# Kernel tuning notes

Measured on AMD Instinct MI355X. Metric: run time of the kernel, lower is better.

## Reference

```python
import jax, jax.numpy as jnp
import numpy as np

# TISA RBF basis (helpers l2_dist / rbf_basis in the repo): f_i(d) = a_i * exp(-|b_i| * (d - c_i)^2)

def setup_inputs() -> dict:
    key = jax.random.key(0)
    k = jax.random.split(key, 8)
    B, L, H, D, S, F = 2, 2048, 8, 64, 2, 5
    qs = jax.random.normal(k[0], (B, L, H, D), dtype=jnp.float32)
    ks = jax.random.normal(k[1], (B, L, H, D), dtype=jnp.float32)
    vs = jax.random.normal(k[2], (B, L, H, D), dtype=jnp.float32)
    qs_s = jax.random.uniform(k[3], (B, L, S), dtype=jnp.float32)
    ks_s = jax.random.uniform(k[4], (B, L, S), dtype=jnp.float32)
    a = jax.random.uniform(k[5], (H * F,), dtype=jnp.float32)
    b = jax.random.uniform(k[6], (H * F,), dtype=jnp.float32)
    c = jax.random.normal(k[7], (H * F,), dtype=jnp.float32) * 0.5
    return {"qs": qs, "ks": ks, "vs": vs, "qs_s": qs_s, "ks_s": ks_s, "a": a, "b": b, "c": c}


def _tisa_attention(qs, ks, vs, qs_s, ks_s, a, b, c):
    B, Q, H, D = qs.shape
    F = a.size // H
    aH, bH, cH = (p.reshape(H, F) for p in (a, b, c))
    # pairwise euclidean distance between query and key locations: [B, Q, K]
    diff = qs_s[:, :, None, :] - ks_s[:, None, :, :]
    d = jnp.sqrt(jnp.sum(diff * diff, axis=-1))
    d_ = d[:, None]  # [B, 1, Q, K] broadcast over heads
    # RBF bias summed over F basis functions (small fixed F -> python sum avoids B,H,F,Q,K blowup)
    bias = sum(
        aH[:, f][None, :, None, None]
        * jnp.exp(-jnp.abs(bH[:, f])[None, :, None, None] * (d_ - cH[:, f][None, :, None, None]) ** 2)
        for f in range(F)
    )  # [B, H, Q, K]
    scale = 1.0 / jnp.sqrt(jnp.asarray(D, dtype=qs.dtype))
    scores = jnp.einsum('bqhd,bkhd->bhqk', qs * scale, ks) + bias
    attn = jax.nn.softmax(scores, axis=-1)
    return jnp.einsum('bhqk,bkhd->bqhd', attn, vs)


def reference(qs, ks, vs, qs_s, ks_s, a, b, c):
    # Matches scan_tisa_biased_attention: online-softmax chunking is mathematically
    # identical to a single stable softmax over the full key axis.
    return _tisa_attention(qs, ks, vs, qs_s, ks_s, a, b, c)
```

## Files before the change

### kernel.cpp

```cpp
#include <hip/hip_runtime.h>
#include <cmath>

typedef _Float16 half8 __attribute__((ext_vector_type(8)));
typedef _Float16 half4 __attribute__((ext_vector_type(4)));
typedef _Float16 half2v __attribute__((ext_vector_type(2)));
typedef __fp16 fp16x2 __attribute__((ext_vector_type(2)));
typedef float f32x4 __attribute__((ext_vector_type(4)));
typedef float f32x2 __attribute__((ext_vector_type(2)));

#define B_ 2
#define L_ 2048
#define H_ 8
#define D_ 64
#define S_ 2
#define F_ 5
#define LUTN 2048
#define LSCALE 1448.1547f
#define LOG2E 1.44269504f
#define QSC (0.125f * LOG2E)

#define QOFF 0
#define KOFF 2097152
#define VOFF 4194304
#define SOFFH 6291456
#define WS_NEED 12615680

#define OFF_K0 0
#define OFF_K1 16384
#define OFF_V0 32768
#define OFF_V1 49152
#define OFF_LUT 65536
#define ARENA_SZ 73744
#define SLOTF (16 * 68 + 16)

#define GLOBAL_LOAD_LDS16(g, l)                                                  \
  __builtin_amdgcn_global_load_lds((const __attribute__((address_space(1))) void*)(g), \
                                   (__attribute__((address_space(3))) void*)(l), 16, 0, 0)

#define FAST_SQRT(x) __builtin_amdgcn_sqrtf(x)

__global__ __launch_bounds__(512, 4)
void tisa_preproc(const float* __restrict__ qs, const float* __restrict__ ks,
                  const float* __restrict__ vs, const float* __restrict__ ks_s,
                  _Float16* __restrict__ wsh) {
  __shared__ _Float16 Vl[64 * 72];
  const int t = threadIdx.x;
  const int bid = blockIdx.x;
  const int xcd = bid & 7, slot = bid >> 3;
  const int u = slot & 31;
  const int bh = xcd * 2 + (slot >> 5);
  const size_t base = ((size_t)(bh >> 3) * L_ + (size_t)u * 64) * (H_ * D_) + (size_t)(bh & 7) * D_;

  {
    int row = t >> 3, c = t & 7;
    const float* src = qs + base + (size_t)row * 512 + c * 8;
    f32x4 x0 = ((const f32x4*)src)[0], x1 = ((const f32x4*)src)[1];
    half8 hh;
#pragma unroll
    for (int k = 0; k < 4; ++k) { hh[k] = (_Float16)(x0[k] * QSC); hh[k + 4] = (_Float16)(x1[k] * QSC); }
    *(half8*)&wsh[QOFF + ((size_t)bh * 32 + u) * 4096 + row * 64 + (c ^ (row & 7)) * 8] = hh;
  }
  {
    int tile = t >> 8, row = (t >> 3) & 31, c = t & 7;
    const float* src = ks + base + (size_t)(tile * 32 + row) * 512 + c * 8;
    f32x4 x0 = ((const f32x4*)src)[0], x1 = ((const f32x4*)src)[1];
    half8 hh;
#pragma unroll
    for (int k = 0; k < 4; ++k) { hh[k] = (_Float16)x0[k]; hh[k + 4] = (_Float16)x1[k]; }
    *(half8*)&wsh[KOFF + ((size_t)bh * 64 + u * 2 + tile) * 2048 + row * 64 + (c ^ (row & 7)) * 8] = hh;
  }
  if ((bh & 7) == 0 && t < 32) {
    const int b = bh >> 3;
    const float* src = ks_s + ((size_t)b * L_ + u * 64) * 2 + t * 4;
    float* dst = (float*)(wsh + SOFFH) + ((size_t)b * L_ + u * 64) * 2 + t * 4;
    f32x4 x = *(const f32x4*)src;
    x *= LSCALE;
    *(f32x4*)dst = x;
  }
  {
    int key = t >> 3, seg = t & 7;
    const float* src = vs + base + (size_t)key * 512 + seg * 8;
    f32x4 a0 = ((const f32x4*)src)[0], a1 = ((const f32x4*)src)[1];
    half8 h0;
#pragma unroll
    for (int k = 0; k < 4; ++k) { h0[k] = (_Float16)a0[k]; h0[k + 4] = (_Float16)a1[k]; }
    *(half8*)&Vl[key * 72 + seg * 8] = h0;
  }
  __syncthreads();
  {
    int tile = t >> 8, s = (t >> 3) & 31, cp2 = t & 7;
    int d = 2 * s + (cp2 >> 2), kb = (cp2 & 3) * 8;
    half8 hh;
#pragma unroll
    for (int j = 0; j < 8; ++j) {
      int kpj = kb + j;
      int orig = ((kpj >> 2) & 1) * 16 + (kpj >> 3) * 4 + (kpj & 3);
      hh[j] = Vl[(tile * 32 + orig) * 72 + d];
    }
    *(half8*)&wsh[VOFF + ((size_t)bh * 64 + u * 2 + tile) * 2048 + s * 64 + (cp2 ^ (s & 7)) * 8] = hh;
  }
}

__global__ __launch_bounds__(1024, 8)
void tisa_attn_main(const float* __restrict__ qs_s, const float* __restrict__ ap,
                    const float* __restrict__ bp, const float* __restrict__ cp,
                    const _Float16* __restrict__ wsh, float* __restrict__ out) {
  __shared__ __align__(16) char arena[ARENA_SZ];
  float* LUT = (float*)(arena + OFF_LUT);

  const int t = threadIdx.x;
  const int lane = t & 63;
  const int w = t >> 6;
  const int g = w >> 2;
  const int qw = w & 3;
  const int t2 = t & 255;
  const int quad = lane >> 4;
  const int l16 = lane & 15;

  const int bid = blockIdx.x;
  const int xcd = bid & 7, slot = bid >> 3;
  const int qt = slot & 31;
  const int bh = xcd * 2 + (slot >> 5);
  const int h = bh & 7;
  const int b = bh >> 3;
  const int q0 = qt * 64;

  {
    float af[F_], nb[F_], cf[F_];
#pragma unroll
    for (int f = 0; f < F_; ++f) {
      af[f] = ap[h * F_ + f];
      nb[f] = -fabsf(bp[h * F_ + f]);
      cf[f] = cp[h * F_ + f];
    }
    for (int i = t; i <= LUTN; i += 1024) {
      float d = ((float)i + 0.5f) * (1.0f / LSCALE);
      float s = 0.f;
#pragma unroll
      for (int f = 0; f < F_; ++f) {
        float e = d - cf[f];
        s += af[f] * __expf(nb[f] * (e * e));
      }
      LUT[i] = (s - 8.0f) * LOG2E;
    }
  }

  const float qx = qs_s[((size_t)b * L_ + q0 + qw * 16 + l16) * 2 + 0] * LSCALE;
  const float qy = qs_s[((size_t)b * L_ + q0 + qw * 16 + l16) * 2 + 1] * LSCALE;

  const _Float16* Qt = wsh + QOFF + ((size_t)bh * 32 + qt) * 4096;
  const _Float16* Kbh = wsh + KOFF + (size_t)bh * 64 * 2048;
  const _Float16* Vbh = wsh + VOFF + (size_t)bh * 64 * 2048;
  const float* wsS = (const float*)(wsh + SOFFH);

  const _Float16* ksrc = Kbh + (size_t)(g * 16) * 2048 + t2 * 8;
  const _Float16* vsrc = Vbh + (size_t)(g * 16) * 2048 + t2 * 8;
  const float* sbase = wsS + ((size_t)b * L_ + g * 512 + quad * 4) * 2;

  if (w < 8)
    GLOBAL_LOAD_LDS16(Qt + w * 512 + lane * 8, arena + OFF_K1 + w * 1024);
  GLOBAL_LOAD_LDS16(ksrc, arena + OFF_K0 + g * 4096 + qw * 1024);
  GLOBAL_LOAD_LDS16(vsrc, arena + OFF_V0 + g * 4096 + qw * 1024);
  ksrc += 2048; vsrc += 2048;
  __syncthreads();

  half8 qA[2];
#pragma unroll
  for (int kb = 0; kb < 2; ++kb)
    qA[kb] = *(const half8*)(arena + OFF_K1 + (qw * 16 + l16) * 128 +
                             ((kb * 4 + quad) ^ (l16 & 7)) * 16);
  __syncthreads();

  f32x4 oc[4];
#pragma unroll
  for (int df = 0; df < 4; ++df) oc[df] = (f32x4){0.f, 0.f, 0.f, 0.f};
  f32x4 lsacc = (f32x4){0.f, 0.f, 0.f, 0.f};
  half8 onesv;
#pragma unroll
  for (int j = 0; j < 8; ++j) onesv[j] = (_Float16)1.0f;

  int cur16 = 0;
  for (int it = 0; it < 16; ++it) {
    const int nxt16 = cur16 ^ 16384;
    if (it < 15) {
      GLOBAL_LOAD_LDS16(ksrc, arena + OFF_K0 + nxt16 + g * 4096 + qw * 1024);
      GLOBAL_LOAD_LDS16(vsrc, arena + OFF_V0 + nxt16 + g * 4096 + qw * 1024);
      ksrc += 2048; vsrc += 2048;
    }

    const float* sit = sbase + it * 64;
    f32x4 c01a = *(const f32x4*)(sit);
    f32x4 c23a = *(const f32x4*)(sit + 4);
    f32x4 c01b = *(const f32x4*)(sit + 32);
    f32x4 c23b = *(const f32x4*)(sit + 36);

    f32x4 acc[2];
#pragma unroll
    for (int nf = 0; nf < 2; ++nf) {
      f32x4 a = (f32x4){0.f, 0.f, 0.f, 0.f};
#pragma unroll
      for (int kb = 0; kb < 2; ++kb) {
        half8 kf = *(const half8*)(arena + OFF_K0 + cur16 + g * 4096 + (nf * 16 + l16) * 128 +
                                   ((kb * 4 + quad) ^ (l16 & 7)) * 16);
        a = __builtin_amdgcn_mfma_f32_16x16x32_f16(kf, qA[kb], a, 0, 0, 0);
      }
      acc[nf] = a;
    }

    float parr[8];
#pragma unroll
    for (int nf = 0; nf < 2; ++nf) {
      f32x4 cA = (nf == 0) ? c01a : c01b;
      f32x4 cB = (nf == 0) ? c23a : c23b;
      float kxr[4] = {cA.x, cA.z, cB.x, cB.z};
      float kyr[4] = {cA.y, cA.w, cB.y, cB.w};
#pragma unroll
      for (int r = 0; r < 4; ++r) {
        float dx = qx - kxr[r], dy = qy - kyr[r];
        float tt = FAST_SQRT(fmaf(dx, dx, dy * dy));
        int ii = (int)tt;
        parr[nf * 4 + r] = __builtin_amdgcn_exp2f(acc[nf][r] + LUT[ii]);
      }
    }
    union { half8 h8; fp16x2 h2[4]; } pu;
#pragma unroll
    for (int k = 0; k < 4; ++k)
      pu.h2[k] = __builtin_amdgcn_cvt_pkrtz(parr[2 * k], parr[2 * k + 1]);
    half8 pw = pu.h8;

    lsacc = __builtin_amdgcn_mfma_f32_16x16x32_f16(pw, onesv, lsacc, 0, 0, 0);
#pragma unroll
    for (int df = 0; df < 4; ++df) {
      half8 vf = *(const half8*)(arena + OFF_V0 + cur16 + g * 4096 + (l16 >> 1) * 128 + df * 1024 +
                                 ((((l16 & 1) * 4 + quad) ^ ((l16 >> 1) & 7)) * 16));
      oc[df] = __builtin_amdgcn_mfma_f32_16x16x32_f16(pw, vf, oc[df], 0, 0, 0);
    }

    __syncthreads();
    cur16 = nxt16;
  }

  float lred[4];
#pragma unroll
  for (int r = 0; r < 4; ++r) lred[r] = lsacc[r];
  __syncthreads();
  float* slots = (float*)arena;
  if (g >= 2) {
    float* sl = slots + ((g - 2) * 4 + qw) * SLOTF;
#pragma unroll
    for (int df = 0; df < 4; ++df)
#pragma unroll
      for (int r = 0; r < 4; ++r)
        sl[(quad * 4 + r) * 68 + df * 16 + l16] = oc[df][r];
    if (l16 == 0) {
#pragma unroll
      for (int r = 0; r < 4; ++r) sl[16 * 68 + quad * 4 + r] = lred[r];
    }
  }
  __syncthreads();
  if (g < 2) {
    float* sl = slots + (g * 4 + qw) * SLOTF;
#pragma unroll
    for (int df = 0; df < 4; ++df)
#pragma unroll
      for (int r = 0; r < 4; ++r)
        oc[df][r] += sl[(quad * 4 + r) * 68 + df * 16 + l16];
#pragma unroll
    for (int r = 0; r < 4; ++r) lred[r] += sl[16 * 68 + quad * 4 + r];
  }
  if (g == 1) {
    float* sl = slots + (4 + qw) * SLOTF;
#pragma unroll
    for (int df = 0; df < 4; ++df)
#pragma unroll
      for (int r = 0; r < 4; ++r)
        sl[(quad * 4 + r) * 68 + df * 16 + l16] = oc[df][r];
    if (l16 == 0) {
#pragma unroll
      for (int r = 0; r < 4; ++r) sl[16 * 68 + quad * 4 + r] = lred[r];
    }
  }
  __syncthreads();
  if (g == 0) {
    float* sl = slots + (4 + qw) * SLOTF;
    float inv_l[4];
#pragma unroll
    for (int r = 0; r < 4; ++r)
      inv_l[r] = 1.f / (lred[r] + sl[16 * 68 + quad * 4 + r]);
#pragma unroll
    for (int df = 0; df < 4; ++df)
#pragma unroll
      for (int r = 0; r < 4; ++r) {
        int qrow = q0 + qw * 16 + quad * 4 + r;
        float v = oc[df][r] + sl[(quad * 4 + r) * 68 + df * 16 + l16];
        out[((size_t)(b * L_ + qrow)) * (H_ * D_) + h * D_ + df * 16 + l16] = v * inv_l[r];
      }
  }
}

#define KSTR 72
#define PH 72
#define FLUTN 512
#define FLSCALE 362.03867f
__global__ __launch_bounds__(512, 4)
void tisa_attn_fallback(const float* __restrict__ qs, const float* __restrict__ ks,
                        const float* __restrict__ vs, const float* __restrict__ qs_s,
                        const float* __restrict__ ks_s, const float* __restrict__ ap,
                        const float* __restrict__ bp, const float* __restrict__ cp,
                        float* __restrict__ out) {
  __shared__ _Float16 Ks[2][64 * KSTR];
  __shared__ _Float16 VT[2][D_ * KSTR];
  __shared__ _Float16 Pf[8][16 * PH];
  __shared__ float kss2[2][64 * 2];
  __shared__ f32x2 LUT2s[FLUTN + 1];
  __shared__ float comb[4][16][64];
  __shared__ float combl[4][16];

  const int t = threadIdx.x;
  const int lane = t & 63;
  const int w = t >> 6;
  const int g = w >> 2;
  const int qw = w & 3;
  const int t2 = t & 255;
  const int quad = lane >> 4;
  const int l16 = lane & 15;
  const int qt = blockIdx.x & 31;
  const int bh = blockIdx.x >> 5;
  const int h = bh & 7;
  const int b = bh >> 3;
  const int q0 = qt * 64;

  float af[F_], nb[F_], cf[F_];
#pragma unroll
  for (int f = 0; f < F_; ++f) {
    af[f] = ap[h * F_ + f];
    nb[f] = -fabsf(bp[h * F_ + f]);
    cf[f] = cp[h * F_ + f];
  }
  for (int i = t; i <= FLUTN; i += 512) {
    float d0 = (float)i * (1.0f / FLSCALE), d1 = (float)(i + 1) * (1.0f / FLSCALE);
    float s0 = 0.f, s1 = 0.f;
#pragma unroll
    for (int f = 0; f < F_; ++f) {
      float e0 = d0 - cf[f], e1 = d1 - cf[f];
      s0 += af[f] * __expf(nb[f] * (e0 * e0));
      s1 += af[f] * __expf(nb[f] * (e1 * e1));
    }
    LUT2s[i] = (f32x2){s0 - 8.0f, s1 - 8.0f};
  }
  float qx[4], qy[4];
#pragma unroll
  for (int r = 0; r < 4; ++r) {
    int qrow = q0 + qw * 16 + quad * 4 + r;
    qx[r] = qs_s[(b * L_ + qrow) * S_ + 0];
    qy[r] = qs_s[(b * L_ + qrow) * S_ + 1];
  }
  if (t < 256) {
    const int row = t >> 2, dc = (t & 3) * 16;
    const float* src = qs + (((size_t)(b * L_ + q0 + row)) * H_ + h) * D_ + dc;
    const f32x4* s4 = (const f32x4*)src;
    f32x4 v0 = s4[0], v1 = s4[1], v2 = s4[2], v3 = s4[3];
    half8 w0, w1;
#pragma unroll
    for (int u = 0; u < 4; ++u) {
      w0[u] = (_Float16)(v0[u] * 0.125f); w0[u + 4] = (_Float16)(v1[u] * 0.125f);
      w1[u] = (_Float16)(v2[u] * 0.125f); w1[u + 4] = (_Float16)(v3[u] * 0.125f);
    }
    *(half8*)&Ks[0][row * KSTR + dc] = w0;
    *(half8*)&Ks[0][row * KSTR + dc + 8] = w1;
  }
  __syncthreads();
  half8 qA[2];
#pragma unroll
  for (int kb = 0; kb < 2; ++kb)
    qA[kb] = *(const half8*)&Ks[0][(qw * 16 + l16) * KSTR + kb * 32 + quad * 8];
  f32x4 oc[4];
#pragma unroll
  for (int df = 0; df < 4; ++df) oc[df] = (f32x4){0.f, 0.f, 0.f, 0.f};
  float l_r[4] = {0.f, 0.f, 0.f, 0.f};

  for (int it = 0; it < 16; ++it) {
    const int k0 = (g * 16 + it) * 64;
    __syncthreads();
    {
      const int row = t2 >> 2, dc = (t2 & 3) * 16;
      const float* src = ks + (((size_t)(b * L_ + k0 + row)) * H_ + h) * D_ + dc;
      const f32x4* s4 = (const f32x4*)src;
      f32x4 v0 = s4[0], v1 = s4[1], v2 = s4[2], v3 = s4[3];
      half8 w0, w1;
#pragma unroll
      for (int u = 0; u < 4; ++u) {
        w0[u] = (_Float16)v0[u]; w0[u + 4] = (_Float16)v1[u];
        w1[u] = (_Float16)v2[u]; w1[u + 4] = (_Float16)v3[u];
      }
      *(half8*)&Ks[g][row * KSTR + dc] = w0;
      *(half8*)&Ks[g][row * KSTR + dc + 8] = w1;
    }
    {
      const int kk = (t2 & 31) * 2, dg = (t2 >> 5) * 8;
      const float* s0 = vs + (((size_t)(b * L_ + k0 + kk)) * H_ + h) * D_ + dg;
      const float* s1 = s0 + H_ * D_;
      f32x4 a0 = ((const f32x4*)s0)[0], a1 = ((const f32x4*)s0)[1];
      f32x4 b0 = ((const f32x4*)s1)[0], b1 = ((const f32x4*)s1)[1];
#pragma unroll
      for (int u = 0; u < 4; ++u) {
        half2v p0 = {(_Float16)a0[u], (_Float16)b0[u]};
        *(half2v*)&VT[g][(dg + u) * KSTR + kk] = p0;
        half2v p1 = {(_Float16)a1[u], (_Float16)b1[u]};
        *(half2v*)&VT[g][(dg + 4 + u) * KSTR + kk] = p1;
      }
    }
    if (t2 < 128) kss2[g][t2] = ks_s[((size_t)(b * L_) + k0 + (t2 >> 1)) * S_ + (t2 & 1)];
    __syncthreads();
    f32x4 acc[4];
#pragma unroll
    for (int nf = 0; nf < 4; ++nf) {
      f32x4 a = (f32x4){0.f, 0.f, 0.f, 0.f};
#pragma unroll
      for (int kb = 0; kb < 2; ++kb) {
        half8 kf = *(const half8*)&Ks[g][(nf * 16 + l16) * KSTR + kb * 32 + quad * 8];
        a = __builtin_amdgcn_mfma_f32_16x16x32_f16(qA[kb], kf, a, 0, 0, 0);
      }
      acc[nf] = a;
    }
#pragma unroll
    for (int nf = 0; nf < 4; ++nf) {
      float kx = kss2[g][(nf * 16 + l16) * 2 + 0];
      float ky = kss2[g][(nf * 16 + l16) * 2 + 1];
#pragma unroll
      for (int r = 0; r < 4; ++r) {
        float dx = qx[r] - kx, dy = qy[r] - ky;
        float dist = FAST_SQRT(fmaf(dx, dx, dy * dy));
        float tt = dist * FLSCALE;
        int ii = (int)tt;
        float fr = tt - (float)ii;
        f32x2 lh = LUT2s[ii];
        float p = __expf(acc[nf][r] + fmaf(fr, lh.y - lh.x, lh.x));
        acc[nf][r] = p;
      }
    }
#pragma unroll
    for (int r = 0; r < 4; ++r)
      l_r[r] += (acc[0][r] + acc[1][r]) + (acc[2][r] + acc[3][r]);
#pragma unroll
    for (int nf = 0; nf < 4; ++nf)
#pragma unroll
      for (int r = 0; r < 4; ++r)
        Pf[w][(quad * 4 + r) * PH + nf * 16 + l16] = (_Float16)acc[nf][r];
#pragma unroll
    for (int kb = 0; kb < 2; ++kb) {
      half8 pa = *(const half8*)&Pf[w][l16 * PH + kb * 32 + quad * 8];
#pragma unroll
      for (int df = 0; df < 4; ++df) {
        half8 vf = *(const half8*)&VT[g][(df * 16 + l16) * KSTR + kb * 32 + quad * 8];
        oc[df] = __builtin_amdgcn_mfma_f32_16x16x32_f16(pa, vf, oc[df], 0, 0, 0);
      }
    }
  }
  __syncthreads();
  float lred[4];
#pragma unroll
  for (int r = 0; r < 4; ++r) {
    float s = l_r[r];
    s += __shfl_xor(s, 1); s += __shfl_xor(s, 2);
    s += __shfl_xor(s, 4); s += __shfl_xor(s, 8);
    lred[r] = s;
  }
  if (g == 1) {
#pragma unroll
    for (int df = 0; df < 4; ++df)
#pragma unroll
      for (int r = 0; r < 4; ++r)
        comb[qw][quad * 4 + r][df * 16 + l16] = oc[df][r];
    if (l16 == 0) {
#pragma unroll
      for (int r = 0; r < 4; ++r) combl[qw][quad * 4 + r] = lred[r];
    }
  }
  __syncthreads();
  if (g == 0) {
    float inv_l[4];
#pragma unroll
    for (int r = 0; r < 4; ++r)
      inv_l[r] = 1.f / (lred[r] + combl[qw][quad * 4 + r]);
#pragma unroll
    for (int df = 0; df < 4; ++df)
#pragma unroll
      for (int r = 0; r < 4; ++r) {
        int qrow = q0 + qw * 16 + quad * 4 + r;
        float v = oc[df][r] + combl[qw][quad * 4 + r] * 0.f + comb[qw][quad * 4 + r][df * 16 + l16];
        out[(((size_t)(b * L_ + qrow)) * H_ + h) * D_ + df * 16 + l16] = v * inv_l[r];
      }
  }
}

extern "C" void kernel_launch(void* const* d_in, const int* in_sizes, int n_in,
                              void* d_out, int out_size, void* d_ws, size_t ws_size,
                              hipStream_t stream) {
  const float* qs = (const float*)d_in[0];
  const float* ks = (const float*)d_in[1];
  const float* vs = (const float*)d_in[2];
  const float* qs_s = (const float*)d_in[3];
  const float* ks_s = (const float*)d_in[4];
  const float* ap = (const float*)d_in[5];
  const float* bp = (const float*)d_in[6];
  const float* cp = (const float*)d_in[7];
  float* out = (float*)d_out;

  if (ws_size >= (size_t)WS_NEED) {
    _Float16* wsh = (_Float16*)d_ws;
    tisa_preproc<<<dim3(512), dim3(512), 0, stream>>>(qs, ks, vs, ks_s, wsh);
    tisa_attn_main<<<dim3(512), dim3(1024), 0, stream>>>(qs_s, ap, bp, cp, wsh, out);
  } else {
    tisa_attn_fallback<<<dim3(512), dim3(512), 0, stream>>>(qs, ks, vs, qs_s, ks_s, ap, bp, cp, out);
  }
}
```

Measured before the change: 129.4 us.

## Precompute pairwise distance LUT indices in preprocessing and drop in-loop sqrt

```diff
diff --git a/kernel.cpp b/kernel.cpp
--- a/kernel.cpp
+++ b/kernel.cpp
@@ -5,6 +5,7 @@
 typedef _Float16 half4 __attribute__((ext_vector_type(4)));
 typedef _Float16 half2v __attribute__((ext_vector_type(2)));
 typedef __fp16 fp16x2 __attribute__((ext_vector_type(2)));
+typedef unsigned short ushort8 __attribute__((ext_vector_type(8)));
 typedef float f32x4 __attribute__((ext_vector_type(4)));
 typedef float f32x2 __attribute__((ext_vector_type(2)));
 
@@ -22,6 +23,9 @@
 #define QOFF 0
 #define KOFF 2097152
 #define VOFF 4194304
+#define IOFF 6291456
+#define WS_NEED2 29360128
+
 #define SOFFH 6291456
 #define WS_NEED 12615680
 
@@ -38,6 +42,276 @@
                                    (__attribute__((address_space(3))) void*)(l), 16, 0, 0)
 
 #define FAST_SQRT(x) __builtin_amdgcn_sqrtf(x)
+
+__global__ __launch_bounds__(256, 4)
+void tisa_preproc2(const float* __restrict__ qs, const float* __restrict__ ks,
+                   const float* __restrict__ vs, const float* __restrict__ qs_s,
+                   const float* __restrict__ ks_s, _Float16* __restrict__ wsh) {
+  const int t = threadIdx.x;
+  const int bid = blockIdx.x;
+  if (bid < 1024) {
+    __shared__ _Float16 Vl[32 * 72];
+    const int xcd = bid & 7, slot = bid >> 3;
+    const int u = slot & 31;
+    const int p = (slot >> 5) & 1;
+    const int bh = xcd * 2 + (slot >> 6);
+    const size_t base = ((size_t)(bh >> 3) * L_ + (size_t)u * 64) * (H_ * D_) + (size_t)(bh & 7) * D_;
+
+    {
+      int row = p * 32 + (t >> 3), c = t & 7;
+      const float* src = qs + base + (size_t)row * 512 + c * 8;
+      f32x4 x0 = ((const f32x4*)src)[0], x1 = ((const f32x4*)src)[1];
+      half8 hh;
+#pragma unroll
+      for (int k = 0; k < 4; ++k) { hh[k] = (_Float16)(x0[k] * QSC); hh[k + 4] = (_Float16)(x1[k] * QSC); }
+      *(half8*)&wsh[QOFF + ((size_t)bh * 32 + u) * 4096 + row * 64 + (c ^ (row & 7)) * 8] = hh;
+    }
+    {
+      int row = t >> 3, c = t & 7;
+      const float* src = ks + base + (size_t)(p * 32 + row) * 512 + c * 8;
+      f32x4 x0 = ((const f32x4*)src)[0], x1 = ((const f32x4*)src)[1];
+      half8 hh;
+#pragma unroll
+      for (int k = 0; k < 4; ++k) { hh[k] = (_Float16)x0[k]; hh[k + 4] = (_Float16)x1[k]; }
+      *(half8*)&wsh[KOFF + ((size_t)bh * 64 + u * 2 + p) * 2048 + row * 64 + (c ^ (row & 7)) * 8] = hh;
+    }
+    {
+      int key = t >> 3, seg = t & 7;
+      const float* src = vs + base + (size_t)(p * 32 + key) * 512 + seg * 8;
+      f32x4 a0 = ((const f32x4*)src)[0], a1 = ((const f32x4*)src)[1];
+      half8 h0;
+#pragma unroll
+      for (int k = 0; k < 4; ++k) { h0[k] = (_Float16)a0[k]; h0[k + 4] = (_Float16)a1[k]; }
+      *(half8*)&Vl[key * 72 + seg * 8] = h0;
+    }
+    __syncthreads();
+    {
+      int s = t >> 3, cp2 = t & 7;
+      int d = 2 * s + (cp2 >> 2), kb = (cp2 & 3) * 8;
+      half8 hh;
+#pragma unroll
+      for (int j = 0; j < 8; ++j) {
+        int kpj = kb + j;
+        int orig = ((kpj >> 2) & 1) * 16 + (kpj >> 3) * 4 + (kpj & 3);
+        hh[j] = Vl[orig * 72 + d];
+      }
+      *(half8*)&wsh[VOFF + ((size_t)bh * 64 + u * 2 + p) * 2048 + s * 64 + (cp2 ^ (s & 7)) * 8] = hh;
+    }
+  } else {
+    __shared__ float kco[64];
+    const int bid2 = bid - 1024;
+    const int kt = bid2 & 63;
+    const int qt = (bid2 >> 6) & 31;
+    const int b = bid2 >> 11;
+    if (t < 16) {
+      f32x4 x = *(const f32x4*)(ks_s + ((size_t)b * L_ + kt * 32) * 2 + t * 4);
+      x *= LSCALE;
+      *(f32x4*)&kco[t * 4] = x;
+    }
+    __syncthreads();
+    const int q = t >> 2, quad = t & 3;
+    f32x2 qc = *(const f32x2*)(qs_s + ((size_t)b * L_ + qt * 64 + q) * 2);
+    const float qxv = qc.x * LSCALE, qyv = qc.y * LSCALE;
+    ushort8 ow;
+#pragma unroll
+    for (int nf = 0; nf < 2; ++nf)
+#pragma unroll
+      for (int r = 0; r < 4; ++r) {
+        int kl = nf * 16 + quad * 4 + r;
+        float dx = qxv - kco[kl * 2], dy = qyv - kco[kl * 2 + 1];
+        float tt = FAST_SQRT(fmaf(dx, dx, dy * dy));
+        ow[nf * 4 + r] = (unsigned short)(((int)tt) << 2);
+      }
+    unsigned short* idx = (unsigned short*)(wsh + IOFF);
+    *(ushort8*)(idx + ((((size_t)b * 32 + qt) * 64 + kt) * 64 + q) * 32 + quad * 8) = ow;
+  }
+}
+
+__global__ __launch_bounds__(1024, 8)
+void tisa_attn_main2(const float* __restrict__ ap, const float* __restrict__ bp,
+                     const float* __restrict__ cp, const _Float16* __restrict__ wsh,
+                     float* __restrict__ out) {
+  __shared__ __align__(16) char arena[ARENA_SZ];
+  float* LUT = (float*)(arena + OFF_LUT);
+
+  const int t = threadIdx.x;
+  const int lane = t & 63;
+  const int w = t >> 6;
+  const int g = w >> 2;
+  const int qw = w & 3;
+  const int t2 = t & 255;
+  const int quad = lane >> 4;
+  const int l16 = lane & 15;
+
+  const int bid = blockIdx.x;
+  const int xcd = bid & 7, slot = bid >> 3;
+  const int qt = slot & 31;
+  const int bh = xcd * 2 + (slot >> 5);
+  const int h = bh & 7;
+  const int b = bh >> 3;
+  const int q0 = qt * 64;
+
+  {
+    float af[F_], nb[F_], cf[F_];
+#pragma unroll
+    for (int f = 0; f < F_; ++f) {
+      af[f] = ap[h * F_ + f];
+      nb[f] = -fabsf(bp[h * F_ + f]);
+      cf[f] = cp[h * F_ + f];
+    }
+    for (int i = t; i <= LUTN; i += 1024) {
+      float d = ((float)i + 0.5f) * (1.0f / LSCALE);
+      float s = 0.f;
+#pragma unroll
+      for (int f = 0; f < F_; ++f) {
+        float e = d - cf[f];
+        s += af[f] * __expf(nb[f] * (e * e));
+      }
+      LUT[i] = (s - 8.0f) * LOG2E;
+    }
+  }
+
+  const _Float16* Qt = wsh + QOFF + ((size_t)bh * 32 + qt) * 4096;
+  const _Float16* Kbh = wsh + KOFF + (size_t)bh * 64 * 2048;
+  const _Float16* Vbh = wsh + VOFF + (size_t)bh * 64 * 2048;
+
+  const _Float16* ksrc = Kbh + (size_t)(g * 16) * 2048 + t2 * 8;
+  const _Float16* vsrc = Vbh + (size_t)(g * 16) * 2048 + t2 * 8;
+  const unsigned short* ivp = (const unsigned short*)(wsh + IOFF) +
+      ((((size_t)b * 32 + qt) * 64 + g * 16) * 64 + (qw * 16 + l16)) * 32 + quad * 8;
+
+  if (w < 8)
+    GLOBAL_LOAD_LDS16(Qt + w * 512 + lane * 8, arena + OFF_K1 + w * 1024);
+  GLOBAL_LOAD_LDS16(ksrc, arena + OFF_K0 + g * 4096 + qw * 1024);
+  GLOBAL_LOAD_LDS16(vsrc, arena + OFF_V0 + g * 4096 + qw * 1024);
+  ksrc += 2048; vsrc += 2048;
+  ushort8 iv = *(const ushort8*)(ivp);
+  __syncthreads();
+
+  half8 qA[2];
+#pragma unroll
+  for (int kb = 0; kb < 2; ++kb)
+    qA[kb] = *(const half8*)(arena + OFF_K1 + (qw * 16 + l16) * 128 +
+                             ((kb * 4 + quad) ^ (l16 & 7)) * 16);
+  __syncthreads();
+
+  f32x4 oc[4];
+#pragma unroll
+  for (int df = 0; df < 4; ++df) oc[df] = (f32x4){0.f, 0.f, 0.f, 0.f};
+  f32x4 lsacc = (f32x4){0.f, 0.f, 0.f, 0.f};
+  half8 onesv;
+#pragma unroll
+  for (int j = 0; j < 8; ++j) onesv[j] = (_Float16)1.0f;
+
+  int cur16 = 0;
+  for (int it = 0; it < 16; ++it) {
+    const int nxt16 = cur16 ^ 16384;
+    if (it < 15) {
+      GLOBAL_LOAD_LDS16(ksrc, arena + OFF_K0 + nxt16 + g * 4096 + qw * 1024);
+      GLOBAL_LOAD_LDS16(vsrc, arena + OFF_V0 + nxt16 + g * 4096 + qw * 1024);
+      ksrc += 2048; vsrc += 2048;
+    }
+    const int itn = (it < 15) ? it + 1 : it;
+    ushort8 ivn = *(const ushort8*)(ivp + (size_t)itn * 2048);
+
+    f32x4 acc[2];
+#pragma unroll
+    for (int nf = 0; nf < 2; ++nf) {
+      f32x4 a = (f32x4){0.f, 0.f, 0.f, 0.f};
+#pragma unroll
+      for (int kb = 0; kb < 2; ++kb) {
+        half8 kf = *(const half8*)(arena + OFF_K0 + cur16 + g * 4096 + (nf * 16 + l16) * 128 +
+                                   ((kb * 4 + quad) ^ (l16 & 7)) * 16);
+        a = __builtin_amdgcn_mfma_f32_16x16x32_f16(kf, qA[kb], a, 0, 0, 0);
+      }
+      acc[nf] = a;
+    }
+
+    float parr[8];
+#pragma unroll
+    for (int nf = 0; nf < 2; ++nf)
+#pragma unroll
+      for (int r = 0; r < 4; ++r) {
+        int j = nf * 4 + r;
+        float bias = *(const float*)((const char*)LUT + (int)iv[j]);
+        parr[j] = __builtin_amdgcn_exp2f(acc[nf][r] + bias);
+      }
+    union { half8 h8; fp16x2 h2[4]; } pu;
+#pragma unroll
+    for (int k = 0; k < 4; ++k)
+      pu.h2[k] = __builtin_amdgcn_cvt_pkrtz(parr[2 * k], parr[2 * k + 1]);
+    half8 pw = pu.h8;
+
+    lsacc = __builtin_amdgcn_mfma_f32_16x16x32_f16(pw, onesv, lsacc, 0, 0, 0);
+#pragma unroll
+    for (int df = 0; df < 4; ++df) {
+      half8 vf = *(const half8*)(arena + OFF_V0 + cur16 + g * 4096 + (l16 >> 1) * 128 + df * 1024 +
+                                 ((((l16 & 1) * 4 + quad) ^ ((l16 >> 1) & 7)) * 16));
+      oc[df] = __builtin_amdgcn_mfma_f32_16x16x32_f16(pw, vf, oc[df], 0, 0, 0);
+    }
+
+    __syncthreads();
+    iv = ivn;
+    cur16 = nxt16;
+  }
+
+  float lred[4];
+#pragma unroll
+  for (int r = 0; r < 4; ++r) lred[r] = lsacc[r];
+  __syncthreads();
+  float* slots = (float*)arena;
+  if (g >= 2) {
+    float* sl = slots + ((g - 2) * 4 + qw) * SLOTF;
+#pragma unroll
+    for (int df = 0; df < 4; ++df)
+#pragma unroll
+      for (int r = 0; r < 4; ++r)
+        sl[(quad * 4 + r) * 68 + df * 16 + l16] = oc[df][r];
+    if (l16 == 0) {
+#pragma unroll
+      for (int r = 0; r < 4; ++r) sl[16 * 68 + quad * 4 + r] = lred[r];
+    }
+  }
+  __syncthreads();
+  if (g < 2) {
+    float* sl = slots + (g * 4 + qw) * SLOTF;
+#pragma unroll
+    for (int df = 0; df < 4; ++df)
+#pragma unroll
+      for (int r = 0; r < 4; ++r)
+        oc[df][r] += sl[(quad * 4 + r) * 68 + df * 16 + l16];
+#pragma unroll
+    for (int r = 0; r < 4; ++r) lred[r] += sl[16 * 68 + quad * 4 + r];
+  }
+  if (g == 1) {
+    float* sl = slots + (4 + qw) * SLOTF;
+#pragma unroll
+    for (int df = 0; df < 4; ++df)
+#pragma unroll
+      for (int r = 0; r < 4; ++r)
+        sl[(quad * 4 + r) * 68 + df * 16 + l16] = oc[df][r];
+    if (l16 == 0) {
+#pragma unroll
+      for (int r = 0; r < 4; ++r) sl[16 * 68 + quad * 4 + r] = lred[r];
+    }
+  }
+  __syncthreads();
+  if (g == 0) {
+    float* sl = slots + (4 + qw) * SLOTF;
+    float inv_l[4];
+#pragma unroll
+    for (int r = 0; r < 4; ++r)
+      inv_l[r] = 1.f / (lred[r] + sl[16 * 68 + quad * 4 + r]);
+#pragma unroll
+    for (int df = 0; df < 4; ++df)
+#pragma unroll
+      for (int r = 0; r < 4; ++r) {
+        int qrow = q0 + qw * 16 + quad * 4 + r;
+        float v = oc[df][r] + sl[(quad * 4 + r) * 68 + df * 16 + l16];
+        out[((size_t)(b * L_ + qrow)) * (H_ * D_) + h * D_ + df * 16 + l16] = v * inv_l[r];
+      }
+  }
+}
 
 __global__ __launch_bounds__(512, 4)
 void tisa_preproc(const float* __restrict__ qs, const float* __restrict__ ks,
@@ -50,7 +324,6 @@
   const int u = slot & 31;
   const int bh = xcd * 2 + (slot >> 5);
   const size_t base = ((size_t)(bh >> 3) * L_ + (size_t)u * 64) * (H_ * D_) + (size_t)(bh & 7) * D_;
-
   {
     int row = t >> 3, c = t & 7;
     const float* src = qs + base + (size_t)row * 512 + c * 8;
@@ -107,7 +380,6 @@
                     const _Float16* __restrict__ wsh, float* __restrict__ out) {
   __shared__ __align__(16) char arena[ARENA_SZ];
   float* LUT = (float*)(arena + OFF_LUT);
-
   const int t = threadIdx.x;
   const int lane = t & 63;
   const int w = t >> 6;
@@ -116,7 +388,6 @@
   const int t2 = t & 255;
   const int quad = lane >> 4;
   const int l16 = lane & 15;
-
   const int bid = blockIdx.x;
   const int xcd = bid & 7, slot = bid >> 3;
   const int qt = slot & 31;
@@ -124,7 +395,6 @@
   const int h = bh & 7;
   const int b = bh >> 3;
   const int q0 = qt * 64;
-
   {
     float af[F_], nb[F_], cf[F_];
 #pragma unroll
@@ -144,33 +414,27 @@
       LUT[i] = (s - 8.0f) * LOG2E;
     }
   }
-
   const float qx = qs_s[((size_t)b * L_ + q0 + qw * 16 + l16) * 2 + 0] * LSCALE;
   const float qy = qs_s[((size_t)b * L_ + q0 + qw * 16 + l16) * 2 + 1] * LSCALE;
-
   const _Float16* Qt = wsh + QOFF + ((size_t)bh * 32 + qt) * 4096;
   const _Float16* Kbh = wsh + KOFF + (size_t)bh * 64 * 2048;
   const _Float16* Vbh = wsh + VOFF + (size_t)bh * 64 * 2048;
   const float* wsS = (const float*)(wsh + SOFFH);
-
   const _Float16* ksrc = Kbh + (size_t)(g * 16) * 2048 + t2 * 8;
   const _Float16* vsrc = Vbh + (size_t)(g * 16) * 2048 + t2 * 8;
   const float* sbase = wsS + ((size_t)b * L_ + g * 512 + quad * 4) * 2;
-
   if (w < 8)
     GLOBAL_LOAD_LDS16(Qt + w * 512 + lane * 8, arena + OFF_K1 + w * 1024);
   GLOBAL_LOAD_LDS16(ksrc, arena + OFF_K0 + g * 4096 + qw * 1024);
   GLOBAL_LOAD_LDS16(vsrc, arena + OFF_V0 + g * 4096 + qw * 1024);
   ksrc += 2048; vsrc += 2048;
   __syncthreads();
-
   half8 qA[2];
 #pragma unroll
   for (int kb = 0; kb < 2; ++kb)
     qA[kb] = *(const half8*)(arena + OFF_K1 + (qw * 16 + l16) * 128 +
                              ((kb * 4 + quad) ^ (l16 & 7)) * 16);
   __syncthreads();
-
   f32x4 oc[4];
 #pragma unroll
   for (int df = 0; df < 4; ++df) oc[df] = (f32x4){0.f, 0.f, 0.f, 0.f};
@@ -178,7 +442,6 @@
   half8 onesv;
 #pragma unroll
   for (int j = 0; j < 8; ++j) onesv[j] = (_Float16)1.0f;
-
   int cur16 = 0;
   for (int it = 0; it < 16; ++it) {
     const int nxt16 = cur16 ^ 16384;
@@ -187,13 +450,11 @@
       GLOBAL_LOAD_LDS16(vsrc, arena + OFF_V0 + nxt16 + g * 4096 + qw * 1024);
       ksrc += 2048; vsrc += 2048;
     }
-
     const float* sit = sbase + it * 64;
     f32x4 c01a = *(const f32x4*)(sit);
     f32x4 c23a = *(const f32x4*)(sit + 4);
     f32x4 c01b = *(const f32x4*)(sit + 32);
     f32x4 c23b = *(const f32x4*)(sit + 36);
-
     f32x4 acc[2];
 #pragma unroll
     for (int nf = 0; nf < 2; ++nf) {
@@ -206,7 +467,6 @@
       }
       acc[nf] = a;
     }
-
     float parr[8];
 #pragma unroll
     for (int nf = 0; nf < 2; ++nf) {
@@ -227,7 +487,6 @@
     for (int k = 0; k < 4; ++k)
       pu.h2[k] = __builtin_amdgcn_cvt_pkrtz(parr[2 * k], parr[2 * k + 1]);
     half8 pw = pu.h8;
-
     lsacc = __builtin_amdgcn_mfma_f32_16x16x32_f16(pw, onesv, lsacc, 0, 0, 0);
 #pragma unroll
     for (int df = 0; df < 4; ++df) {
@@ -235,11 +494,9 @@
                                  ((((l16 & 1) * 4 + quad) ^ ((l16 >> 1) & 7)) * 16));
       oc[df] = __builtin_amdgcn_mfma_f32_16x16x32_f16(pw, vf, oc[df], 0, 0, 0);
     }
-
     __syncthreads();
     cur16 = nxt16;
   }
-
   float lred[4];
 #pragma unroll
   for (int r = 0; r < 4; ++r) lred[r] = lsacc[r];
@@ -507,7 +764,11 @@
   const float* cp = (const float*)d_in[7];
   float* out = (float*)d_out;
 
-  if (ws_size >= (size_t)WS_NEED) {
+  if (ws_size >= (size_t)WS_NEED2) {
+    _Float16* wsh = (_Float16*)d_ws;
+    tisa_preproc2<<<dim3(5120), dim3(256), 0, stream>>>(qs, ks, vs, qs_s, ks_s, wsh);
+    tisa_attn_main2<<<dim3(512), dim3(1024), 0, stream>>>(ap, bp, cp, wsh, out);
+  } else if (ws_size >= (size_t)WS_NEED) {
     _Float16* wsh = (_Float16*)d_ws;
     tisa_preproc<<<dim3(512), dim3(512), 0, stream>>>(qs, ks, vs, ks_s, wsh);
     tisa_attn_main<<<dim3(512), dim3(1024), 0, stream>>>(qs_s, ap, bp, cp, wsh, out);
```

New measurement: 146.3 us. 1.13x slower.

## Halve main kernel block size so each wave handles two query subtiles, reusing K/V fragments

Applied to the files above, without the earlier changes.

```diff
diff --git a/kernel.cpp b/kernel.cpp
--- a/kernel.cpp
+++ b/kernel.cpp
@@ -39,11 +39,12 @@
 
 #define FAST_SQRT(x) __builtin_amdgcn_sqrtf(x)
 
+#define VLS 74
 __global__ __launch_bounds__(512, 4)
 void tisa_preproc(const float* __restrict__ qs, const float* __restrict__ ks,
                   const float* __restrict__ vs, const float* __restrict__ ks_s,
                   _Float16* __restrict__ wsh) {
-  __shared__ _Float16 Vl[64 * 72];
+  __shared__ _Float16 Vl[64 * VLS];
   const int t = threadIdx.x;
   const int bid = blockIdx.x;
   const int xcd = bid & 7, slot = bid >> 3;
@@ -84,7 +85,7 @@
     half8 h0;
 #pragma unroll
     for (int k = 0; k < 4; ++k) { h0[k] = (_Float16)a0[k]; h0[k + 4] = (_Float16)a1[k]; }
-    *(half8*)&Vl[key * 72 + seg * 8] = h0;
+    *(half8*)&Vl[key * VLS + seg * 8] = h0;
   }
   __syncthreads();
   {
@@ -95,13 +96,13 @@
     for (int j = 0; j < 8; ++j) {
       int kpj = kb + j;
       int orig = ((kpj >> 2) & 1) * 16 + (kpj >> 3) * 4 + (kpj & 3);
-      hh[j] = Vl[(tile * 32 + orig) * 72 + d];
+      hh[j] = Vl[(tile * 32 + orig) * VLS + d];
     }
     *(half8*)&wsh[VOFF + ((size_t)bh * 64 + u * 2 + tile) * 2048 + s * 64 + (cp2 ^ (s & 7)) * 8] = hh;
   }
 }
 
-__global__ __launch_bounds__(1024, 8)
+__global__ __launch_bounds__(512, 4)
 void tisa_attn_main(const float* __restrict__ qs_s, const float* __restrict__ ap,
                     const float* __restrict__ bp, const float* __restrict__ cp,
                     const _Float16* __restrict__ wsh, float* __restrict__ out) {
@@ -111,9 +112,9 @@
   const int t = threadIdx.x;
   const int lane = t & 63;
   const int w = t >> 6;
-  const int g = w >> 2;
-  const int qw = w & 3;
-  const int t2 = t & 255;
+  const int g = w >> 1;
+  const int qh = w & 1;
+  const int tg = t & 127;
   const int quad = lane >> 4;
   const int l16 = lane & 15;
 
@@ -133,7 +134,7 @@
       nb[f] = -fabsf(bp[h * F_ + f]);
       cf[f] = cp[h * F_ + f];
     }
-    for (int i = t; i <= LUTN; i += 1024) {
+    for (int i = t; i <= LUTN; i += 512) {
       float d = ((float)i + 0.5f) * (1.0f / LSCALE);
       float s = 0.f;
 #pragma unroll
@@ -145,36 +146,49 @@
     }
   }
 
-  const float qx = qs_s[((size_t)b * L_ + q0 + qw * 16 + l16) * 2 + 0] * LSCALE;
-  const float qy = qs_s[((size_t)b * L_ + q0 + qw * 16 + l16) * 2 + 1] * LSCALE;
+  float qx[2], qy[2];
+#pragma unroll
+  for (int s = 0; s < 2; ++s) {
+    qx[s] = qs_s[((size_t)b * L_ + q0 + (qh * 2 + s) * 16 + l16) * 2 + 0] * LSCALE;
+    qy[s] = qs_s[((size_t)b * L_ + q0 + (qh * 2 + s) * 16 + l16) * 2 + 1] * LSCALE;
+  }
 
   const _Float16* Qt = wsh + QOFF + ((size_t)bh * 32 + qt) * 4096;
   const _Float16* Kbh = wsh + KOFF + (size_t)bh * 64 * 2048;
   const _Float16* Vbh = wsh + VOFF + (size_t)bh * 64 * 2048;
   const float* wsS = (const float*)(wsh + SOFFH);
 
-  const _Float16* ksrc = Kbh + (size_t)(g * 16) * 2048 + t2 * 8;
-  const _Float16* vsrc = Vbh + (size_t)(g * 16) * 2048 + t2 * 8;
+  const _Float16* ksrc = Kbh + (size_t)(g * 16) * 2048 + tg * 8;
+  const _Float16* vsrc = Vbh + (size_t)(g * 16) * 2048 + tg * 8;
+  char* kdst = arena + OFF_K0 + g * 4096 + qh * 1024;
+  char* vdst = arena + OFF_V0 + g * 4096 + qh * 1024;
   const float* sbase = wsS + ((size_t)b * L_ + g * 512 + quad * 4) * 2;
 
-  if (w < 8)
-    GLOBAL_LOAD_LDS16(Qt + w * 512 + lane * 8, arena + OFF_K1 + w * 1024);
-  GLOBAL_LOAD_LDS16(ksrc, arena + OFF_K0 + g * 4096 + qw * 1024);
-  GLOBAL_LOAD_LDS16(vsrc, arena + OFF_V0 + g * 4096 + qw * 1024);
+  GLOBAL_LOAD_LDS16(Qt + w * 512 + lane * 8, arena + OFF_K1 + w * 1024);
+  GLOBAL_LOAD_LDS16(ksrc, kdst);
+  GLOBAL_LOAD_LDS16(ksrc + 1024, kdst + 2048);
+  GLOBAL_LOAD_LDS16(vsrc, vdst);
+  GLOBAL_LOAD_LDS16(vsrc + 1024, vdst + 2048);
   ksrc += 2048; vsrc += 2048;
   __syncthreads();
 
-  half8 qA[2];
-#pragma unroll
-  for (int kb = 0; kb < 2; ++kb)
-    qA[kb] = *(const half8*)(arena + OFF_K1 + (qw * 16 + l16) * 128 +
-                             ((kb * 4 + quad) ^ (l16 & 7)) * 16);
-  __syncthreads();
-
-  f32x4 oc[4];
-#pragma unroll
-  for (int df = 0; df < 4; ++df) oc[df] = (f32x4){0.f, 0.f, 0.f, 0.f};
-  f32x4 lsacc = (f32x4){0.f, 0.f, 0.f, 0.f};
+  half8 qA[2][2];
+#pragma unroll
+  for (int s = 0; s < 2; ++s)
+#pragma unroll
+    for (int kb = 0; kb < 2; ++kb)
+      qA[s][kb] = *(const half8*)(arena + OFF_K1 + ((qh * 2 + s) * 16 + l16) * 128 +
+                                  ((kb * 4 + quad) ^ (l16 & 7)) * 16);
+  __syncthreads();
+
+  f32x4 oc[2][4];
+#pragma unroll
+  for (int s = 0; s < 2; ++s)
+#pragma unroll
+    for (int df = 0; df < 4; ++df) oc[s][df] = (f32x4){0.f, 0.f, 0.f, 0.f};
+  f32x4 lsacc[2];
+  lsacc[0] = (f32x4){0.f, 0.f, 0.f, 0.f};
+  lsacc[1] = (f32x4){0.f, 0.f, 0.f, 0.f};
   half8 onesv;
 #pragma unroll
   for (int j = 0; j < 8; ++j) onesv[j] = (_Float16)1.0f;
@@ -183,118 +197,139 @@
   for (int it = 0; it < 16; ++it) {
     const int nxt16 = cur16 ^ 16384;
     if (it < 15) {
-      GLOBAL_LOAD_LDS16(ksrc, arena + OFF_K0 + nxt16 + g * 4096 + qw * 1024);
-      GLOBAL_LOAD_LDS16(vsrc, arena + OFF_V0 + nxt16 + g * 4096 + qw * 1024);
+      GLOBAL_LOAD_LDS16(ksrc, kdst + nxt16);
+      GLOBAL_LOAD_LDS16(ksrc + 1024, kdst + nxt16 + 2048);
+      GLOBAL_LOAD_LDS16(vsrc, vdst + nxt16);
+      GLOBAL_LOAD_LDS16(vsrc + 1024, vdst + nxt16 + 2048);
       ksrc += 2048; vsrc += 2048;
     }
 
     const float* sit = sbase + it * 64;
-    f32x4 c01a = *(const f32x4*)(sit);
-    f32x4 c23a = *(const f32x4*)(sit + 4);
-    f32x4 c01b = *(const f32x4*)(sit + 32);
-    f32x4 c23b = *(const f32x4*)(sit + 36);
-
-    f32x4 acc[2];
-#pragma unroll
-    for (int nf = 0; nf < 2; ++nf) {
-      f32x4 a = (f32x4){0.f, 0.f, 0.f, 0.f};
-#pragma unroll
-      for (int kb = 0; kb < 2; ++kb) {
-        half8 kf = *(const half8*)(arena + OFF_K0 + cur16 + g * 4096 + (nf * 16 + l16) * 128 +
-                                   ((kb * 4 + quad) ^ (l16 & 7)) * 16);
-        a = __builtin_amdgcn_mfma_f32_16x16x32_f16(kf, qA[kb], a, 0, 0, 0);
-      }
-      acc[nf] = a;
-    }
-
-    float parr[8];
-#pragma unroll
-    for (int nf = 0; nf < 2; ++nf) {
-      f32x4 cA = (nf == 0) ? c01a : c01b;
-      f32x4 cB = (nf == 0) ? c23a : c23b;
-      float kxr[4] = {cA.x, cA.z, cB.x, cB.z};
-      float kyr[4] = {cA.y, cA.w, cB.y, cB.w};
-#pragma unroll
-      for (int r = 0; r < 4; ++r) {
-        float dx = qx - kxr[r], dy = qy - kyr[r];
+    f32x4 cA = *(const f32x4*)(sit);
+    f32x4 cB = *(const f32x4*)(sit + 4);
+    f32x4 cC = *(const f32x4*)(sit + 32);
+    f32x4 cD = *(const f32x4*)(sit + 36);
+    float kx[8] = {cA.x, cA.z, cB.x, cB.z, cC.x, cC.z, cD.x, cD.z};
+    float ky[8] = {cA.y, cA.w, cB.y, cB.w, cC.y, cC.w, cD.y, cD.w};
+
+    half8 kf[2][2];
+#pragma unroll
+    for (int nf = 0; nf < 2; ++nf)
+#pragma unroll
+      for (int kb = 0; kb < 2; ++kb)
+        kf[nf][kb] = *(const half8*)(arena + OFF_K0 + cur16 + g * 4096 +
+                                     (nf * 16 + l16) * 128 + ((kb * 4 + quad) ^ (l16 & 7)) * 16);
+    f32x4 acc[2][2];
+#pragma unroll
+    for (int s = 0; s < 2; ++s)
+#pragma unroll
+      for (int nf = 0; nf < 2; ++nf) {
+        f32x4 a = (f32x4){0.f, 0.f, 0.f, 0.f};
+        a = __builtin_amdgcn_mfma_f32_16x16x32_f16(kf[nf][0], qA[s][0], a, 0, 0, 0);
+        a = __builtin_amdgcn_mfma_f32_16x16x32_f16(kf[nf][1], qA[s][1], a, 0, 0, 0);
+        acc[s][nf] = a;
+      }
+
+    half8 pw[2];
+#pragma unroll
+    for (int s = 0; s < 2; ++s) {
+      float parr[8];
+#pragma unroll
+      for (int j = 0; j < 8; ++j) {
+        float dx = qx[s] - kx[j], dy = qy[s] - ky[j];
         float tt = FAST_SQRT(fmaf(dx, dx, dy * dy));
-        int ii = (int)tt;
-        parr[nf * 4 + r] = __builtin_amdgcn_exp2f(acc[nf][r] + LUT[ii]);
-      }
-    }
-    union { half8 h8; fp16x2 h2[4]; } pu;
-#pragma unroll
-    for (int k = 0; k < 4; ++k)
-      pu.h2[k] = __builtin_amdgcn_cvt_pkrtz(parr[2 * k], parr[2 * k + 1]);
-    half8 pw = pu.h8;
-
-    lsacc = __builtin_amdgcn_mfma_f32_16x16x32_f16(pw, onesv, lsacc, 0, 0, 0);
+        parr[j] = __builtin_amdgcn_exp2f(acc[s][j >> 2][j & 3] + LUT[(int)tt]);
+      }
+      union { half8 h8; fp16x2 h2[4]; } pu;
+#pragma unroll
+      for (int k = 0; k < 4; ++k)
+        pu.h2[k] = __builtin_amdgcn_cvt_pkrtz(parr[2 * k], parr[2 * k + 1]);
+      pw[s] = pu.h8;
+    }
+
+    lsacc[0] = __builtin_amdgcn_mfma_f32_16x16x32_f16(pw[0], onesv, lsacc[0], 0, 0, 0);
+    lsacc[1] = __builtin_amdgcn_mfma_f32_16x16x32_f16(pw[1], onesv, lsacc[1], 0, 0, 0);
 #pragma unroll
     for (int df = 0; df < 4; ++df) {
       half8 vf = *(const half8*)(arena + OFF_V0 + cur16 + g * 4096 + (l16 >> 1) * 128 + df * 1024 +
                                  ((((l16 & 1) * 4 + quad) ^ ((l16 >> 1) & 7)) * 16));
-      oc[df] = __builtin_amdgcn_mfma_f32_16x16x32_f16(pw, vf, oc[df], 0, 0, 0);
+      oc[0][df] = __builtin_amdgcn_mfma_f32_16x16x32_f16(pw[0], vf, oc[0][df], 0, 0, 0);
+      oc[1][df] = __builtin_amdgcn_mfma_f32_16x16x32_f16(pw[1], vf, oc[1][df], 0, 0, 0);
     }
 
     __syncthreads();
     cur16 = nxt16;
   }
 
-  float lred[4];
-#pragma unroll
-  for (int r = 0; r < 4; ++r) lred[r] = lsacc[r];
+  float lred[2][4];
+#pragma unroll
+  for (int s = 0; s < 2; ++s)
+#pragma unroll
+    for (int r = 0; r < 4; ++r) lred[s][r] = lsacc[s][r];
   __syncthreads();
   float* slots = (float*)arena;
   if (g >= 2) {
-    float* sl = slots + ((g - 2) * 4 + qw) * SLOTF;
-#pragma unroll
-    for (int df = 0; df < 4; ++df)
+#pragma unroll
+    for (int s = 0; s < 2; ++s) {
+      float* sl = slots + ((g - 2) * 4 + qh * 2 + s) * SLOTF;
+#pragma unroll
+      for (int df = 0; df < 4; ++df)
+#pragma unroll
+        for (int r = 0; r < 4; ++r)
+          sl[(quad * 4 + r) * 68 + df * 16 + l16] = oc[s][df][r];
+      if (l16 == 0) {
+#pragma unroll
+        for (int r = 0; r < 4; ++r) sl[16 * 68 + quad * 4 + r] = lred[s][r];
+      }
+    }
+  }
+  __syncthreads();
+  if (g < 2) {
+#pragma unroll
+    for (int s = 0; s < 2; ++s) {
+      float* sl = slots + (g * 4 + qh * 2 + s) * SLOTF;
+#pragma unroll
+      for (int df = 0; df < 4; ++df)
+#pragma unroll
+        for (int r = 0; r < 4; ++r)
+          oc[s][df][r] += sl[(quad * 4 + r) * 68 + df * 16 + l16];
+#pragma unroll
+      for (int r = 0; r < 4; ++r) lred[s][r] += sl[16 * 68 + quad * 4 + r];
+    }
+  }
+  if (g == 1) {
+#pragma unroll
+    for (int s = 0; s < 2; ++s) {
+      float* sl = slots + (4 + qh * 2 + s) * SLOTF;
+#pragma unroll
+      for (int df = 0; df < 4; ++df)
+#pragma unroll
+        for (int r = 0; r < 4; ++r)
+          sl[(quad * 4 + r) * 68 + df * 16 + l16] = oc[s][df][r];
+      if (l16 == 0) {
+#pragma unroll
+        for (int r = 0; r < 4; ++r) sl[16 * 68 + quad * 4 + r] = lred[s][r];
+      }
+    }
+  }
+  __syncthreads();
+  if (g == 0) {
+#pragma unroll
+    for (int s = 0; s < 2; ++s) {
+      float* sl = slots + (4 + qh * 2 + s) * SLOTF;
+      float inv_l[4];
 #pragma unroll
       for (int r = 0; r < 4; ++r)
-        sl[(quad * 4 + r) * 68 + df * 16 + l16] = oc[df][r];
-    if (l16 == 0) {
-#pragma unroll
-      for (int r = 0; r < 4; ++r) sl[16 * 68 + quad * 4 + r] = lred[r];
-    }
-  }
-  __syncthreads();
-  if (g < 2) {
-    float* sl = slots + (g * 4 + qw) * SLOTF;
-#pragma unroll
-    for (int df = 0; df < 4; ++df)
-#pragma unroll
-      for (int r = 0; r < 4; ++r)
-        oc[df][r] += sl[(quad * 4 + r) * 68 + df * 16 + l16];
-#pragma unroll
-    for (int r = 0; r < 4; ++r) lred[r] += sl[16 * 68 + quad * 4 + r];
-  }
-  if (g == 1) {
-    float* sl = slots + (4 + qw) * SLOTF;
-#pragma unroll
-    for (int df = 0; df < 4; ++df)
-#pragma unroll
-      for (int r = 0; r < 4; ++r)
-        sl[(quad * 4 + r) * 68 + df * 16 + l16] = oc[df][r];
-    if (l16 == 0) {
-#pragma unroll
-      for (int r = 0; r < 4; ++r) sl[16 * 68 + quad * 4 + r] = lred[r];
-    }
-  }
-  __syncthreads();
-  if (g == 0) {
-    float* sl = slots + (4 + qw) * SLOTF;
-    float inv_l[4];
-#pragma unroll
-    for (int r = 0; r < 4; ++r)
-      inv_l[r] = 1.f / (lred[r] + sl[16 * 68 + quad * 4 + r]);
-#pragma unroll
-    for (int df = 0; df < 4; ++df)
-#pragma unroll
-      for (int r = 0; r < 4; ++r) {
-        int qrow = q0 + qw * 16 + quad * 4 + r;
-        float v = oc[df][r] + sl[(quad * 4 + r) * 68 + df * 16 + l16];
-        out[((size_t)(b * L_ + qrow)) * (H_ * D_) + h * D_ + df * 16 + l16] = v * inv_l[r];
-      }
+        inv_l[r] = 1.f / (lred[s][r] + sl[16 * 68 + quad * 4 + r]);
+#pragma unroll
+      for (int df = 0; df < 4; ++df)
+#pragma unroll
+        for (int r = 0; r < 4; ++r) {
+          int qrow = q0 + (qh * 2 + s) * 16 + quad * 4 + r;
+          float v = oc[s][df][r] + sl[(quad * 4 + r) * 68 + df * 16 + l16];
+          out[((size_t)(b * L_ + qrow)) * (H_ * D_) + h * D_ + df * 16 + l16] = v * inv_l[r];
+        }
+    }
   }
 }
 
@@ -510,7 +545,7 @@
   if (ws_size >= (size_t)WS_NEED) {
     _Float16* wsh = (_Float16*)d_ws;
     tisa_preproc<<<dim3(512), dim3(512), 0, stream>>>(qs, ks, vs, ks_s, wsh);
-    tisa_attn_main<<<dim3(512), dim3(1024), 0, stream>>>(qs_s, ap, bp, cp, wsh, out);
+    tisa_attn_main<<<dim3(512), dim3(512), 0, stream>>>(qs_s, ap, bp, cp, wsh, out);
   } else {
     tisa_attn_fallback<<<dim3(512), dim3(512), 0, stream>>>(qs, ks, vs, qs_s, ks_s, ap, bp, cp, out);
   }
```

Measured after the change: 123.1 us. 4.9% less time.
